# Kernel tuning notes

Hardware: AMD Instinct MI355X
Metric: run time of the kernel (lower is better)

## Reference

```python
import jax, jax.numpy as jnp
import numpy as np

D_MODEL = 1024
NUM_HEADS = 16
HEAD_DIM = D_MODEL // NUM_HEADS


def setup_inputs() -> dict:
    key = jax.random.key(0)
    ks = jax.random.split(key, 8)
    B, L, D = 4, 4096, D_MODEL
    s = 1.0 / np.sqrt(D)
    return {
        "x": jax.random.normal(ks[0], (B, L, D), dtype=jnp.float32),
        "y": jax.random.normal(ks[1], (B, L, D), dtype=jnp.float32),
        "Wkv": jax.random.normal(ks[2], (D, 2 * D), dtype=jnp.float32) * s,
        "bkv": jnp.zeros((2 * D,), dtype=jnp.float32),
        "Wq": jax.random.normal(ks[3], (D, D), dtype=jnp.float32) * s,
        "bq": jnp.zeros((D,), dtype=jnp.float32),
        "Wo": jax.random.normal(ks[4], (D, D), dtype=jnp.float32) * s,
        "bo": jnp.zeros((D,), dtype=jnp.float32),
    }


def reference(x, y, Wkv, bkv, Wq, bq, Wo, bo):
    B, L, D = x.shape
    H, hd = NUM_HEADS, HEAD_DIM
    # projections (torch Linear: x @ W^T + b; here W stored as [in,out])
    kv = (x @ Wkv + bkv).reshape(B, L, H, 2 * hd)
    q = (y @ Wq + bq).reshape(B, L, H, hd)
    # NOTE: source's permute() results are discarded, so attention is taken
    # over the HEADS axis at each position: attn shape [B, L, H, H].
    k, v = jnp.split(kv, 2, axis=-1)  # each [B, L, H, hd]
    scale = 1.0 / np.sqrt(hd)
    attn = jnp.einsum("blhd,blgd->blhg", q, k) * scale  # [B,L,H,H]
    attn = jax.nn.softmax(attn, axis=-1)
    val = jnp.einsum("blhg,blgd->blhd", attn, v).reshape(B, L, D)
    return val @ Wo + bo
```

## Files before the change

### kernel.cpp

```cpp
#include <hip/hip_runtime.h>
#include <math.h>


typedef __attribute__((ext_vector_type(8))) short bf16x8;
typedef __attribute__((ext_vector_type(4))) float f32x4;
typedef __attribute__((ext_vector_type(16))) float f32x16;

__device__ __forceinline__ float b2f(short s) {
    union { unsigned u; float f; } x;
    x.u = ((unsigned)(unsigned short)s) << 16;
    return x.f;
}
__device__ __forceinline__ short f2b(float f) {
    union { float f; unsigned u; } x;
    x.f = f;
    unsigned r = (x.u + 0x7FFFu + ((x.u >> 16) & 1u)) >> 16;
    return (short)r;
}

__global__ __launch_bounds__(256) void cast2_f32_bf16(
    const float* __restrict__ in0, short* __restrict__ out0,
    const float* __restrict__ in1, short* __restrict__ out1, int n) {
    int i = (blockIdx.x * 256 + threadIdx.x) * 4;
    const float* in = in0;
    short* out = out0;
    if (i >= n) {
        i -= n;
        in = in1;
        out = out1;
    }
    float4 v = *(const float4*)(in + i);
    short4 o;
    o.x = f2b(v.x); o.y = f2b(v.y); o.z = f2b(v.z); o.w = f2b(v.w);
    *(short4*)(out + i) = o;
}

__global__ __launch_bounds__(256) void transpose_cast2(
    const float* __restrict__ W0, short* __restrict__ Wt0,
    const float* __restrict__ W1, short* __restrict__ Wt1, int K, int N) {
    const float* W = blockIdx.z ? W1 : W0;
    short* Wt = blockIdx.z ? Wt1 : Wt0;
    __shared__ float tile[32][33];
    int tx = threadIdx.x;
    int ty = threadIdx.y;
    int bx = blockIdx.x * 32;
    int by = blockIdx.y * 32;
#pragma unroll
    for (int j = 0; j < 32; j += 8)
        tile[ty + j][tx] = W[(size_t)(by + ty + j) * N + bx + tx];
    __syncthreads();
#pragma unroll
    for (int j = 0; j < 32; j += 8)
        Wt[(size_t)(bx + ty + j) * K + by + tx] = f2b(tile[tx][ty + j]);
}

#define BM 256
#define BN 256

#define GLD16(g, l)                                           \
    __builtin_amdgcn_global_load_lds(                         \
        (const __attribute__((address_space(1))) void*)(g),   \
        (__attribute__((address_space(3))) void*)(l), 16, 0, 0)

template <int OUT_BF16>
__global__ __launch_bounds__(512, 2) void gemm_bt(
    const short* __restrict__ A,
    const short* __restrict__ Bt,
    const float* __restrict__ bias,
    void* __restrict__ Cout,
    int M, int N, int K) {
    __shared__ __align__(16) short lds[65536];

    const int tid = threadIdx.x;

    const int NX = gridDim.x;
    const int nwg = NX * gridDim.y;
    int lin = blockIdx.y * NX + blockIdx.x;
    lin = (lin & 7) * (nwg >> 3) + (lin >> 3);
    const int bn = (lin % NX) * BN;
    const int bm = (lin / NX) * BM;

    const int lane = tid & 63;
    const int wave = tid >> 6;
    const int wr = wave >> 2;
    const int wc = wave & 3;
    const int l31 = lane & 31;
    const int kh = lane >> 5;
    const int u = (l31 >> 1) & 3;
    const int s0 = ((u + (kh << 1)) & 3) << 3;
    const int s1 = ((u + 1 + (kh << 1)) & 3) << 3;
    const int arow = (wr * 128 + l31) * 32;
    const int brow = (wc * 64 + l31) * 32;

    const int srow = tid >> 2;
    {
    }
    const int t_ = tid & 3;
    const int us_ = (tid >> 3) & 3;
    const int d_ = (t_ - us_) & 3;
    const int c_ = (d_ == 1) ? 2 : (d_ == 2 ? 1 : d_);
    const int sslot = c_ * 8;
    const short* agp = A + (size_t)(bm + srow) * K + sslot;
    const short* bgp = Bt + (size_t)(bn + srow) * K + sslot;
    const size_t qstep = (size_t)128 * K;
    char* const lbase = (char*)lds;
    const int dst = tid * 16;

    f32x16 acc[4][2];
#pragma unroll
    for (int i = 0; i < 4; ++i)
#pragma unroll
        for (int j = 0; j < 2; ++j)
#pragma unroll
            for (int e = 0; e < 16; ++e) acc[i][j][e] = 0.f;

#pragma unroll
    for (int h = 0; h < 3; ++h) {
        const int kk = h << 5;
        GLD16(agp + kk, lbase + h * 32768 + dst);
        GLD16(agp + kk + qstep, lbase + h * 32768 + 8192 + dst);
        GLD16(bgp + kk, lbase + h * 32768 + 16384 + dst);
        GLD16(bgp + kk + qstep, lbase + h * 32768 + 24576 + dst);
    }
    asm volatile("s_waitcnt vmcnt(8)" ::: "memory");
    __builtin_amdgcn_s_barrier();

    const int NH = K >> 5;
    for (int mm = 0; mm < NH; mm += 4) {
#pragma unroll
        for (int uu = 0; uu < 4; ++uu) {
            const int m = mm + uu;
            const int slot = uu;
            const int wslot = (uu + 3) & 3;
            const int kis = ((m + 3 < NH) ? (m + 3) : (NH - 1)) << 5;
            const short* la = &lds[slot * 16384 + arow];
            const short* lb = &lds[slot * 16384 + 8192 + brow];
            bf16x8 af0[4], bf0[2], af1[4], bf1[2];
#pragma unroll
            for (int mi = 0; mi < 4; ++mi)
                af0[mi] = *(const bf16x8*)(la + mi * 1024 + s0);
#pragma unroll
            for (int nj = 0; nj < 2; ++nj)
                bf0[nj] = *(const bf16x8*)(lb + nj * 1024 + s0);
            __builtin_amdgcn_sched_barrier(0);
#pragma unroll
            for (int mi = 0; mi < 4; ++mi)
                af1[mi] = *(const bf16x8*)(la + mi * 1024 + s1);
#pragma unroll
            for (int nj = 0; nj < 2; ++nj)
                bf1[nj] = *(const bf16x8*)(lb + nj * 1024 + s1);
            GLD16(agp + kis, lbase + wslot * 32768 + dst);
            GLD16(agp + kis + qstep, lbase + wslot * 32768 + 8192 + dst);
            GLD16(bgp + kis, lbase + wslot * 32768 + 16384 + dst);
            GLD16(bgp + kis + qstep, lbase + wslot * 32768 + 24576 + dst);
            asm volatile("s_waitcnt lgkmcnt(6)" ::: "memory");
            __builtin_amdgcn_sched_barrier(0);
            __builtin_amdgcn_s_setprio(1);
#pragma unroll
            for (int mi = 0; mi < 4; ++mi)
#pragma unroll
                for (int nj = 0; nj < 2; ++nj)
                    acc[mi][nj] = __builtin_amdgcn_mfma_f32_32x32x16_bf16(
                        af0[mi], bf0[nj], acc[mi][nj], 0, 0, 0);
            asm volatile("s_waitcnt lgkmcnt(0)" ::: "memory");
            __builtin_amdgcn_sched_barrier(0);
#pragma unroll
            for (int mi = 0; mi < 4; ++mi)
#pragma unroll
                for (int nj = 0; nj < 2; ++nj)
                    acc[mi][nj] = __builtin_amdgcn_mfma_f32_32x32x16_bf16(
                        af1[mi], bf1[nj], acc[mi][nj], 0, 0, 0);
            __builtin_amdgcn_s_setprio(0);
            asm volatile("s_waitcnt vmcnt(8)" ::: "memory");
            __builtin_amdgcn_s_barrier();
        }
    }

    float bv[2];
#pragma unroll
    for (int nj = 0; nj < 2; ++nj) bv[nj] = bias[bn + wc * 64 + nj * 32 + l31];
#pragma unroll
    for (int mi = 0; mi < 4; ++mi) {
#pragma unroll
        for (int q = 0; q < 4; ++q) {
#pragma unroll
            for (int rr = 0; rr < 4; ++rr) {
                const int row = bm + wr * 128 + mi * 32 + rr + 8 * q + 4 * kh;
#pragma unroll
                for (int nj = 0; nj < 2; ++nj) {
                    const int col = bn + wc * 64 + nj * 32 + l31;
                    float v = acc[mi][nj][q * 4 + rr] + bv[nj];
                    if (OUT_BF16)
                        ((short*)Cout)[(size_t)row * N + col] = f2b(v);
                    else
                        ((float*)Cout)[(size_t)row * N + col] = v;
                }
            }
        }
    }
    asm volatile("s_waitcnt vmcnt(0)" ::: "memory");
}

__global__ __launch_bounds__(256) void attn_kernel(
    const short* __restrict__ Q, const short* __restrict__ KV,
    short* __restrict__ VAL) {
    const int wave = threadIdx.x >> 6;
    const int lane = threadIdx.x & 63;
    const size_t p = (size_t)blockIdx.x * 4 + wave;
    const int dq = lane & 3;

    const bf16x8* qp = (const bf16x8*)(Q + p * 1024 + (size_t)lane * 16);
    bf16x8 q0 = qp[0], q1 = qp[1];
    float q[16];
#pragma unroll
    for (int j = 0; j < 8; ++j) {
        q[j] = b2f(q0[j]);
        q[8 + j] = b2f(q1[j]);
    }

    const short* kvb = KV + p * 2048;

    float s[16];
#pragma unroll
    for (int g = 0; g < 16; ++g) {
        const bf16x8* kp = (const bf16x8*)(kvb + g * 128 + dq * 16);
        bf16x8 k0 = kp[0], k1 = kp[1];
        float d = 0.f;
#pragma unroll
        for (int j = 0; j < 8; ++j) {
            d += q[j] * b2f(k0[j]);
            d += q[8 + j] * b2f(k1[j]);
        }
        s[g] = d;
    }
    float mx = -1e30f;
#pragma unroll
    for (int g = 0; g < 16; ++g) {
        s[g] += __shfl_xor(s[g], 1, 64);
        s[g] += __shfl_xor(s[g], 2, 64);
        s[g] *= 0.125f;
        mx = fmaxf(mx, s[g]);
    }
    float ssum = 0.f;
#pragma unroll
    for (int g = 0; g < 16; ++g) {
        s[g] = __expf(s[g] - mx);
        ssum += s[g];
    }
    const float inv = 1.0f / ssum;

    float vo[16];
#pragma unroll
    for (int j = 0; j < 16; ++j) vo[j] = 0.f;
#pragma unroll
    for (int g = 0; g < 16; ++g) {
        const float w = s[g] * inv;
        const bf16x8* vp = (const bf16x8*)(kvb + g * 128 + 64 + dq * 16);
        bf16x8 v0 = vp[0], v1 = vp[1];
#pragma unroll
        for (int j = 0; j < 8; ++j) {
            vo[j] += w * b2f(v0[j]);
            vo[8 + j] += w * b2f(v1[j]);
        }
    }

    bf16x8 o0, o1;
#pragma unroll
    for (int j = 0; j < 8; ++j) {
        o0[j] = f2b(vo[j]);
        o1[j] = f2b(vo[8 + j]);
    }
    bf16x8* op = (bf16x8*)(VAL + p * 1024 + (size_t)lane * 16);
    op[0] = o0;
    op[1] = o1;
}

extern "C" void kernel_launch(void* const* d_in, const int* in_sizes, int n_in,
                              void* d_out, int out_size, void* d_ws,
                              size_t ws_size, hipStream_t stream) {
    const float* x = (const float*)d_in[0];
    const float* y = (const float*)d_in[1];
    const float* Wkv = (const float*)d_in[2];
    const float* bkv = (const float*)d_in[3];
    const float* Wq = (const float*)d_in[4];
    const float* bq = (const float*)d_in[5];
    const float* Wo = (const float*)d_in[6];
    const float* bo = (const float*)d_in[7];
    float* out = (float*)d_out;

    const int D = 1024;
    const int M = 16384;

    char* ws = (char*)d_ws;
    short* Xb = (short*)(ws);
    short* Yb = (short*)(ws + 33554432);
    short* Wkvt = (short*)(ws + 67108864);
    short* Wqt = (short*)(ws + 71303168);
    short* Wot = (short*)(ws + 73400320);
    short* KV = (short*)(ws + 75497472);
    short* Q = Xb;
    short* VAL = Yb;

    const int n = M * D;

    cast2_f32_bf16<<<2 * n / 1024, 256, 0, stream>>>(x, Xb, y, Yb, n);
    transpose_cast2<<<dim3(2 * D / 32, D / 32, 1), dim3(32, 8), 0, stream>>>(
        Wkv, Wkvt, (const float*)0, (short*)0, D, 2 * D);
    transpose_cast2<<<dim3(D / 32, D / 32, 2), dim3(32, 8), 0, stream>>>(
        Wq, Wqt, Wo, Wot, D, D);

    gemm_bt<1><<<dim3(2 * D / BN, M / BM), 512, 0, stream>>>(
        Xb, Wkvt, bkv, KV, M, 2 * D, D);
    gemm_bt<1><<<dim3(D / BN, M / BM), 512, 0, stream>>>(
        Yb, Wqt, bq, Q, M, D, D);
    attn_kernel<<<M / 4, 256, 0, stream>>>(Q, KV, VAL);
    gemm_bt<0><<<dim3(D / BN, M / BM), 512, 0, stream>>>(
        VAL, Wot, bo, out, M, D, D);
}
```

Baseline: 377.6 us.

## Restructure GEMM LDS layout to k-octet slabs and split loads into ping-pong phases

Changes the global-to-LDS staging so each thread loads one row's 8-element k-octet, giving a k-major slab layout in LDS that drops the XOR/rotation swizzle arithmetic for fragment reads. The main loop is split into two phases, each issuing half the LDS reads and half the global prefetches followed by MFMAs, with extra s_barriers between phases. This is meant to cut bank conflicts and address math and to interleave memory with compute across waves. The cost is more workgroup barriers per k-step, and the new layout may bring its own LDS bank conflicts.

```diff
diff --git a/kernel.cpp b/kernel.cpp
--- a/kernel.cpp
+++ b/kernel.cpp
@@ -86,23 +86,13 @@
     const int wc = wave & 3;
     const int l31 = lane & 31;
     const int kh = lane >> 5;
-    const int u = (l31 >> 1) & 3;
-    const int s0 = ((u + (kh << 1)) & 3) << 3;
-    const int s1 = ((u + 1 + (kh << 1)) & 3) << 3;
-    const int arow = (wr * 128 + l31) * 32;
-    const int brow = (wc * 64 + l31) * 32;
-
-    const int srow = tid >> 2;
-    {
-    }
-    const int t_ = tid & 3;
-    const int us_ = (tid >> 3) & 3;
-    const int d_ = (t_ - us_) & 3;
-    const int c_ = (d_ == 1) ? 2 : (d_ == 2 ? 1 : d_);
-    const int sslot = c_ * 8;
-    const short* agp = A + (size_t)(bm + srow) * K + sslot;
-    const short* bgp = Bt + (size_t)(bn + srow) * K + sslot;
-    const size_t qstep = (size_t)128 * K;
+    const int abase = kh * 2048 + (wr * 128 + l31) * 8;
+    const int bbase = 8192 + kh * 2048 + (wc * 64 + l31) * 8;
+
+    const int srow = tid & 255;
+    const int soct = (tid >> 8) << 3;
+    const short* agp = A + (size_t)(bm + srow) * K + soct;
+    const short* bgp = Bt + (size_t)(bn + srow) * K + soct;
     char* const lbase = (char*)lds;
     const int dst = tid * 16;
 
@@ -118,9 +108,9 @@
     for (int h = 0; h < 3; ++h) {
         const int kk = h << 5;
         GLD16(agp + kk, lbase + h * 32768 + dst);
-        GLD16(agp + kk + qstep, lbase + h * 32768 + 8192 + dst);
+        GLD16(agp + kk + 16, lbase + h * 32768 + 8192 + dst);
         GLD16(bgp + kk, lbase + h * 32768 + 16384 + dst);
-        GLD16(bgp + kk + qstep, lbase + h * 32768 + 24576 + dst);
+        GLD16(bgp + kk + 16, lbase + h * 32768 + 24576 + dst);
     }
     asm volatile("s_waitcnt vmcnt(8)" ::: "memory");
     __builtin_amdgcn_s_barrier();
@@ -133,27 +123,20 @@
             const int slot = uu;
             const int wslot = (uu + 3) & 3;
             const int kis = ((m + 3 < NH) ? (m + 3) : (NH - 1)) << 5;
-            const short* la = &lds[slot * 16384 + arow];
-            const short* lb = &lds[slot * 16384 + 8192 + brow];
+            const short* la = &lds[slot * 16384 + abase];
+            const short* lb = &lds[slot * 16384 + bbase];
             bf16x8 af0[4], bf0[2], af1[4], bf1[2];
 #pragma unroll
             for (int mi = 0; mi < 4; ++mi)
-                af0[mi] = *(const bf16x8*)(la + mi * 1024 + s0);
+                af0[mi] = *(const bf16x8*)(la + mi * 256);
 #pragma unroll
             for (int nj = 0; nj < 2; ++nj)
-                bf0[nj] = *(const bf16x8*)(lb + nj * 1024 + s0);
+                bf0[nj] = *(const bf16x8*)(lb + nj * 256);
+            GLD16(agp + kis, lbase + wslot * 32768 + dst);
+            GLD16(agp + kis + 16, lbase + wslot * 32768 + 8192 + dst);
             __builtin_amdgcn_sched_barrier(0);
-#pragma unroll
-            for (int mi = 0; mi < 4; ++mi)
-                af1[mi] = *(const bf16x8*)(la + mi * 1024 + s1);
-#pragma unroll
-            for (int nj = 0; nj < 2; ++nj)
-                bf1[nj] = *(const bf16x8*)(lb + nj * 1024 + s1);
-            GLD16(agp + kis, lbase + wslot * 32768 + dst);
-            GLD16(agp + kis + qstep, lbase + wslot * 32768 + 8192 + dst);
-            GLD16(bgp + kis, lbase + wslot * 32768 + 16384 + dst);
-            GLD16(bgp + kis + qstep, lbase + wslot * 32768 + 24576 + dst);
-            asm volatile("s_waitcnt lgkmcnt(6)" ::: "memory");
+            __builtin_amdgcn_s_barrier();
+            asm volatile("s_waitcnt lgkmcnt(0)" ::: "memory");
             __builtin_amdgcn_sched_barrier(0);
             __builtin_amdgcn_s_setprio(1);
 #pragma unroll
@@ -162,8 +145,21 @@
                 for (int nj = 0; nj < 2; ++nj)
                     acc[mi][nj] = __builtin_amdgcn_mfma_f32_32x32x16_bf16(
                         af0[mi], bf0[nj], acc[mi][nj], 0, 0, 0);
+            __builtin_amdgcn_s_setprio(0);
+            __builtin_amdgcn_s_barrier();
+#pragma unroll
+            for (int mi = 0; mi < 4; ++mi)
+                af1[mi] = *(const bf16x8*)(la + 4096 + mi * 256);
+#pragma unroll
+            for (int nj = 0; nj < 2; ++nj)
+                bf1[nj] = *(const bf16x8*)(lb + 4096 + nj * 256);
+            GLD16(bgp + kis, lbase + wslot * 32768 + 16384 + dst);
+            GLD16(bgp + kis + 16, lbase + wslot * 32768 + 24576 + dst);
+            __builtin_amdgcn_sched_barrier(0);
+            __builtin_amdgcn_s_barrier();
             asm volatile("s_waitcnt lgkmcnt(0)" ::: "memory");
             __builtin_amdgcn_sched_barrier(0);
+            __builtin_amdgcn_s_setprio(1);
 #pragma unroll
             for (int mi = 0; mi < 4; ++mi)
 #pragma unroll
```

Result: slower. 435.6 us (+15.4%).
